# Optimization experiments

Measured on AMD Instinct MI355X. Metric: run time of the kernel, lower is better.

## Reference

```python
import jax, jax.numpy as jnp
import numpy as np

OUT_F, IN_F, RANK, GROUP = 8192, 8192, 16, 128
N_GROUPS = OUT_F * IN_F // GROUP  # 524288
TOKENS = 256


def block_dequantize_2bit(weight_q2, weight_norm):
    """weight_q2: [n_groups, GROUP//4] int (uint8 values), weight_norm: [n_groups, 1] fp16.
    Each byte packs 4 two-bit codes little-endian (code k in bits 2k..2k+1).
    Code q in {0..3} dequantizes to ((q/3)*2 - 1) * norm."""
    shifts = jnp.array([0, 2, 4, 6], dtype=jnp.int32)
    q = (weight_q2[:, :, None] >> shifts) & 3          # [n_groups, GROUP//4, 4]
    q = q.reshape(weight_q2.shape[0], -1).astype(jnp.float32)  # [n_groups, GROUP]
    return (q * (2.0 / 3.0) - 1.0) * weight_norm.astype(jnp.float32)


def setup_inputs() -> dict:
    key = jax.random.key(0)
    ks = jax.random.split(key, 6)
    x = jax.random.normal(ks[0], (TOKENS, IN_F), dtype=jnp.float32)
    weight_q2 = jax.random.randint(ks[1], (N_GROUPS, GROUP // 4), 0, 256, dtype=jnp.int32)
    weight_norm = jax.random.uniform(ks[2], (N_GROUPS, 1), dtype=jnp.float16, minval=0.01, maxval=1.0)
    bias = jax.random.normal(ks[3], (OUT_F,), dtype=jnp.float32)
    lora_a = jax.random.normal(ks[4], (RANK, IN_F), dtype=jnp.float32) * 0.02
    lora_b = jax.random.normal(ks[5], (OUT_F, RANK), dtype=jnp.float32) * 0.02
    return {"x": x, "weight_q2": weight_q2, "weight_norm": weight_norm,
            "bias": bias, "lora_a": lora_a, "lora_b": lora_b}


def reference(x, weight_q2, weight_norm, bias, lora_a, lora_b):
    x_f32 = x.astype(jnp.float32)
    W = block_dequantize_2bit(weight_q2, weight_norm).reshape(OUT_F, IN_F)  # fp32 [out, in]
    base_out = x_f32 @ W.T + bias                       # [tokens, out]
    lora_out = (x_f32 @ lora_a.T) @ lora_b.T            # [tokens, out]
    return (base_out + lora_out).astype(x.dtype)
```

## Files before the change

kernel.cpp:

```cpp
#include <hip/hip_runtime.h>
#include <hip/hip_fp16.h>

typedef unsigned int u32;
typedef unsigned short u16;
typedef _Float16 f16x8 __attribute__((ext_vector_type(8)));
typedef float f32x4 __attribute__((ext_vector_type(4)));

#define OUT_F 8192
#define IN_F 8192
#define TOKENS 256
#define N_GROUPS 524288
#define SPLITK 8
#define KSPAN (IN_F / SPLITK)
#define KT (KSPAN / 64)

#define XB_OFF 0
#define T_OFF ((size_t)TOKENS * IN_F * 2)
#define NF_OFF (T_OFF + 65536)
#define PART_OFF (NF_OFF + (size_t)N_GROUPS * 2)
#define PART_BYTES ((size_t)SPLITK * TOKENS * OUT_F * 4)
#define WS_NEED (PART_OFF + PART_BYTES)

#define GLOAD16(g, l)                                                        \
  __builtin_amdgcn_global_load_lds(                                          \
      (const __attribute__((address_space(1))) void*)(g),                    \
      (__attribute__((address_space(3))) void*)(l), 16, 0, 0)

__device__ __forceinline__ u32 hm2(u32 a, __half2 s) {
  return __builtin_bit_cast(u32, __hmul2(__builtin_bit_cast(__half2, a), s));
}

__global__ __launch_bounds__(256) void prep(const void* __restrict__ wn,
                                            __half* __restrict__ nf,
                                            const float* __restrict__ x,
                                            const float* __restrict__ la,
                                            u16* __restrict__ xb,
                                            float* __restrict__ t) {
  int tid = threadIdx.x;
  if (blockIdx.x < 512) {
    __shared__ int votes[3];
    if (tid < 3) votes[tid] = 0;
    __syncthreads();
    const u16* pu = (const u16*)wn;
    const u32* pw = (const u32*)wn;
    int v16 = 0, vbf = 0, vf = 0;
    for (int i = tid; i < 2048; i += 256) {
      u16 u = pu[i];
      float h = __half2float(__builtin_bit_cast(__half, u));
      float b = __builtin_bit_cast(float, ((u32)u) << 16);
      if (h > 0.008f && h < 1.002f) v16++;
      if (b > 0.008f && b < 1.002f) vbf++;
    }
    for (int i = tid; i < 1024; i += 256) {
      float f = __builtin_bit_cast(float, pw[i]);
      if (f > 0.008f && f < 1.002f) vf++;
    }
    atomicAdd(&votes[0], v16);
    atomicAdd(&votes[1], vbf);
    atomicAdd(&votes[2], vf);
    __syncthreads();
    int a16 = votes[0], abf = votes[1], af32 = 2 * votes[2];
    int mode = (a16 >= abf && a16 >= af32) ? 0 : (abf >= af32 ? 1 : 2);
#pragma unroll
    for (int i = 0; i < 4; ++i) {
      int g = blockIdx.x * 1024 + i * 256 + tid;
      float v;
      if (mode == 0) v = __half2float(((const __half*)wn)[g]);
      else if (mode == 1) v = __builtin_bit_cast(float, ((u32)((const u16*)wn)[g]) << 16);
      else v = ((const float*)wn)[g];
      nf[g] = __float2half(v);
    }
    return;
  }
  int b2 = blockIdx.x - 512;
  int m = b2 & 255;
  int half = b2 >> 8;
  const float4* xr = (const float4*)(x + (size_t)m * IN_F);
  u32* xbr = (u32*)(xb + (size_t)m * IN_F);
  float pl[16];
#pragma unroll
  for (int r = 0; r < 16; ++r) pl[r] = 0.f;
#pragma unroll
  for (int it = 0; it < 4; ++it) {
    int k4 = half * 1024 + it * 256 + tid;
    float4 xv = xr[k4];
    u32 p0 = __builtin_bit_cast(u32, __float22half2_rn(make_float2(xv.x, xv.y)));
    u32 p1 = __builtin_bit_cast(u32, __float22half2_rn(make_float2(xv.z, xv.w)));
    ((uint2*)xbr)[k4] = make_uint2(p0, p1);
#pragma unroll
    for (int r = 0; r < 16; ++r) {
      const float4 av = ((const float4*)(la + (size_t)r * IN_F))[k4];
      pl[r] = fmaf(xv.x, av.x, pl[r]);
      pl[r] = fmaf(xv.y, av.y, pl[r]);
      pl[r] = fmaf(xv.z, av.z, pl[r]);
      pl[r] = fmaf(xv.w, av.w, pl[r]);
    }
  }
#pragma unroll
  for (int r = 0; r < 16; ++r) {
    float v = pl[r];
#pragma unroll
    for (int d = 32; d > 0; d >>= 1) v += __shfl_xor(v, d);
    pl[r] = v;
  }
  __shared__ float red[4][16];
  int wave = tid >> 6, lane = tid & 63;
  if (lane == 0) {
#pragma unroll
    for (int r = 0; r < 16; ++r) red[wave][r] = pl[r];
  }
  __syncthreads();
  if (tid < 16)
    t[((size_t)half * TOKENS + m) * 16 + tid] =
        red[0][tid] + red[1][tid] + red[2][tid] + red[3][tid];
}

__global__ __launch_bounds__(256) void prep2(const float* __restrict__ t,
                                             const float* __restrict__ lb,
                                             const float* __restrict__ bias,
                                             float* __restrict__ out) {
  __shared__ float tS[16 * 16];
  int tid = threadIdx.x;
  int n = blockIdx.x * 256 + tid;
  int mbase = blockIdx.y * 16;
  if (tid < 64) {
    float4 a = ((const float4*)(t + (size_t)mbase * 16))[tid];
    float4 b = ((const float4*)(t + (size_t)TOKENS * 16 + (size_t)mbase * 16))[tid];
    ((float4*)tS)[tid] = make_float4(a.x + b.x, a.y + b.y, a.z + b.z, a.w + b.w);
  }
  const float4* lbp = (const float4*)(lb + (size_t)n * 16);
  float4 b0 = lbp[0], b1 = lbp[1], b2 = lbp[2], b3 = lbp[3];
  float bv = bias[n];
  __syncthreads();
#pragma unroll
  for (int mm = 0; mm < 16; ++mm) {
    const float* tr = &tS[mm * 16];
    float a = bv;
    a += tr[0] * b0.x + tr[1] * b0.y + tr[2] * b0.z + tr[3] * b0.w;
    a += tr[4] * b1.x + tr[5] * b1.y + tr[6] * b1.z + tr[7] * b1.w;
    a += tr[8] * b2.x + tr[9] * b2.y + tr[10] * b2.z + tr[11] * b2.w;
    a += tr[12] * b3.x + tr[13] * b3.y + tr[14] * b3.z + tr[15] * b3.w;
    out[(size_t)(mbase + mm) * OUT_F + n] = a;
  }
}

__global__ __launch_bounds__(256) void finish(const float* __restrict__ t,
                                              const float* __restrict__ lb,
                                              const float* __restrict__ bias,
                                              const float* __restrict__ part,
                                              float* __restrict__ out) {
  __shared__ float tS[16 * 16];
  int tid = threadIdx.x;
  int n = blockIdx.x * 256 + tid;
  int mbase = blockIdx.y * 16;
  if (tid < 64) {
    float4 a = ((const float4*)(t + (size_t)mbase * 16))[tid];
    float4 b = ((const float4*)(t + (size_t)TOKENS * 16 + (size_t)mbase * 16))[tid];
    ((float4*)tS)[tid] = make_float4(a.x + b.x, a.y + b.y, a.z + b.z, a.w + b.w);
  }
  const float4* lbp = (const float4*)(lb + (size_t)n * 16);
  float4 b0 = lbp[0], b1 = lbp[1], b2 = lbp[2], b3 = lbp[3];
  float bv = bias[n];
  __syncthreads();
#pragma unroll
  for (int mm = 0; mm < 16; ++mm) {
    const float* tr = &tS[mm * 16];
    float a = bv;
    a += tr[0] * b0.x + tr[1] * b0.y + tr[2] * b0.z + tr[3] * b0.w;
    a += tr[4] * b1.x + tr[5] * b1.y + tr[6] * b1.z + tr[7] * b1.w;
    a += tr[8] * b2.x + tr[9] * b2.y + tr[10] * b2.z + tr[11] * b2.w;
    a += tr[12] * b3.x + tr[13] * b3.y + tr[14] * b3.z + tr[15] * b3.w;
    size_t base = (size_t)(mbase + mm) * OUT_F + n;
#pragma unroll
    for (int kz = 0; kz < SPLITK; ++kz)
      a += part[(size_t)kz * TOKENS * OUT_F + base];
    out[base] = a;
  }
}

__global__ __launch_bounds__(256, 3) void gemm_q2(const u16* __restrict__ xb,
                                                  const int* __restrict__ wq,
                                                  const __half* __restrict__ wn,
                                                  float* __restrict__ dst,
                                                  int mode) {
  __shared__ __align__(16) u16 As[2][128 * 64];
  __shared__ __align__(16) u16 Bs[128 * 64];
  __shared__ uint2 lut[256];

  int tid = threadIdx.x;
  int n0 = blockIdx.x * 128;
  int m0 = blockIdx.y * 128;
  int kz = blockIdx.z;
  int kbase = kz * KSPAN;

  {
    int b = tid;
    float v0 = (float)(b & 3) * (2.f / 3.f) - 1.f;
    float v1 = (float)((b >> 2) & 3) * (2.f / 3.f) - 1.f;
    float v2 = (float)((b >> 4) & 3) * (2.f / 3.f) - 1.f;
    float v3 = (float)((b >> 6) & 3) * (2.f / 3.f) - 1.f;
    u32 lo = __builtin_bit_cast(u32, __float22half2_rn(make_float2(v0, v1)));
    u32 hi = __builtin_bit_cast(u32, __float22half2_rn(make_float2(v2, v3)));
    lut[b] = make_uint2(lo, hi);
  }

  int wave = tid >> 6, lane = tid & 63;
  int quad = lane >> 4, l15 = lane & 15;
  int mo = (wave & 1) * 64, no = (wave >> 1) * 64;

  int aslot[4];
  const u16* ag[4];
#pragma unroll
  for (int i = 0; i < 4; ++i) {
    int s = tid + i * 256;
    int mm = s >> 3, c = s & 7;
    int cl = c ^ (mm & 7);
    aslot[i] = s;
    ag[i] = xb + (size_t)(m0 + mm) * IN_F + kbase + cl * 8;
  }

  int bn = tid >> 1, h = tid & 1;
  const char* gB = (const char*)wq + (size_t)(n0 + bn) * IN_F + kbase + h * 32;
  const __half* wnp = wn + (size_t)(n0 + bn) * 64 + kz * (KSPAN / 128);

  f32x4 zero4 = {0.f, 0.f, 0.f, 0.f};
  f32x4 acc[4][4];
#pragma unroll
  for (int i = 0; i < 4; ++i)
#pragma unroll
    for (int j = 0; j < 4; ++j) acc[i][j] = zero4;

#pragma unroll
  for (int i = 0; i < 4; ++i) GLOAD16(ag[i], &((uint4*)As[0])[aslot[i]]);
  int4 pb0 = *(const int4*)(gB);
  int4 pb1 = *(const int4*)(gB + 16);
  __half pn = wnp[0];
  int cur = 0;

#pragma unroll 1
  for (int kt = 0; kt < KT; ++kt) {
    __syncthreads();

    {
      __half2 nh = __half2half2(pn);
      int vv[8] = {pb0.x, pb0.y, pb0.z, pb0.w, pb1.x, pb1.y, pb1.z, pb1.w};
      u32 uu[16];
#pragma unroll
      for (int e = 0; e < 8; ++e) {
        uint2 lv = lut[vv[e] & 255];
        uu[2 * e] = hm2(lv.x, nh);
        uu[2 * e + 1] = hm2(lv.y, nh);
      }
      uint4* Bw = (uint4*)Bs;
#pragma unroll
      for (int cc = 0; cc < 4; ++cc) {
        int pc = (h * 4 + cc) ^ (bn & 7);
        Bw[bn * 8 + pc] = make_uint4(uu[4 * cc], uu[4 * cc + 1], uu[4 * cc + 2], uu[4 * cc + 3]);
      }
    }

    if (kt < KT - 1) {
      int ko = (kt + 1) * 64;
#pragma unroll
      for (int i = 0; i < 4; ++i)
        GLOAD16(ag[i] + ko, &((uint4*)As[cur ^ 1])[aslot[i]]);
      pb0 = *(const int4*)(gB + ko);
      pb1 = *(const int4*)(gB + ko + 16);
      pn = wnp[(kt + 1) >> 1];
    }

    asm volatile("s_waitcnt lgkmcnt(0)" ::: "memory");
    __builtin_amdgcn_s_barrier();
    asm volatile("" ::: "memory");

    const uint4* Ar = (const uint4*)As[cur];
#pragma unroll
    for (int ks = 0; ks < 2; ++ks) {
      f16x8 af[4], bf[4];
#pragma unroll
      for (int mt = 0; mt < 4; ++mt) {
        int row = mo + mt * 16 + l15;
        int pc = (ks * 4 + quad) ^ (row & 7);
        af[mt] = __builtin_bit_cast(f16x8, Ar[row * 8 + pc]);
      }
#pragma unroll
      for (int nt = 0; nt < 4; ++nt) {
        int row = no + nt * 16 + l15;
        int pc = (ks * 4 + quad) ^ (row & 7);
        bf[nt] = __builtin_bit_cast(f16x8, ((const uint4*)Bs)[row * 8 + pc]);
      }
#pragma unroll
      for (int mt = 0; mt < 4; ++mt)
#pragma unroll
        for (int nt = 0; nt < 4; ++nt)
          acc[mt][nt] = __builtin_amdgcn_mfma_f32_16x16x32_f16(af[mt], bf[nt], acc[mt][nt], 0, 0, 0);
    }
    cur ^= 1;
  }

  if (mode) {
    float* pp = dst + (size_t)kz * TOKENS * OUT_F;
#pragma unroll
    for (int mt = 0; mt < 4; ++mt)
#pragma unroll
      for (int nt = 0; nt < 4; ++nt)
#pragma unroll
        for (int r = 0; r < 4; ++r) {
          int mm = m0 + mo + mt * 16 + quad * 4 + r;
          int nn = n0 + no + nt * 16 + l15;
          pp[(size_t)mm * OUT_F + nn] = acc[mt][nt][r];
        }
  } else {
#pragma unroll
    for (int mt = 0; mt < 4; ++mt)
#pragma unroll
      for (int nt = 0; nt < 4; ++nt)
#pragma unroll
        for (int r = 0; r < 4; ++r) {
          int mm = m0 + mo + mt * 16 + quad * 4 + r;
          int nn = n0 + no + nt * 16 + l15;
          atomicAdd(&dst[(size_t)mm * OUT_F + nn], acc[mt][nt][r]);
        }
  }
}

extern "C" void kernel_launch(void* const* d_in, const int* in_sizes, int n_in,
                              void* d_out, int out_size, void* d_ws, size_t ws_size,
                              hipStream_t stream) {
  (void)in_sizes; (void)n_in; (void)out_size;
  const float* x = (const float*)d_in[0];
  const int* wq = (const int*)d_in[1];
  const void* wn_raw = d_in[2];
  const float* bias = (const float*)d_in[3];
  const float* la = (const float*)d_in[4];
  const float* lb = (const float*)d_in[5];
  float* out = (float*)d_out;

  u16* xb = (u16*)((char*)d_ws + XB_OFF);
  float* t = (float*)((char*)d_ws + T_OFF);
  __half* nf = (__half*)((char*)d_ws + NF_OFF);
  float* part = (float*)((char*)d_ws + PART_OFF);
  int usep = ws_size >= WS_NEED;

  prep<<<1024, 256, 0, stream>>>(wn_raw, nf, x, la, xb, t);
  if (usep) {
    gemm_q2<<<dim3(OUT_F / 128, TOKENS / 128, SPLITK), 256, 0, stream>>>(xb, wq, nf, part, 1);
    finish<<<dim3(OUT_F / 256, TOKENS / 16), 256, 0, stream>>>(t, lb, bias, part, out);
  } else {
    prep2<<<dim3(OUT_F / 256, TOKENS / 16), 256, 0, stream>>>(t, lb, bias, out);
    gemm_q2<<<dim3(OUT_F / 128, TOKENS / 128, SPLITK), 256, 0, stream>>>(xb, wq, nf, out, 0);
  }
}
```

Measured before the change: 185.8 us.

## Triple-buffer A tiles with vmcnt waits, halve split-K, re-tile LoRA prep

The GEMM loop now keeps three LDS buffers for the activation tile. Loads are issued two k-steps ahead and waited on with vmcnt, replacing the earlier double buffer that drained every step. Split-K drops from 8 to 4, which halves the partial-sum traffic in finish, and launch bounds are relaxed to 2 waves per SIMD because LDS use grows. The LoRA prep kernel now gives each block 16 tokens over one eighth of K, producing 8 slices that prep2 and finish sum. The loop issues a wrapped, redundant load on the last iterations, and the lower occupancy may expose more latency.

```diff
diff --git a/kernel.cpp b/kernel.cpp
--- a/kernel.cpp
+++ b/kernel.cpp
@@ -10,13 +10,15 @@
 #define IN_F 8192
 #define TOKENS 256
 #define N_GROUPS 524288
-#define SPLITK 8
+#define SPLITK 4
 #define KSPAN (IN_F / SPLITK)
 #define KT (KSPAN / 64)
+#define TSLICES 8
 
 #define XB_OFF 0
 #define T_OFF ((size_t)TOKENS * IN_F * 2)
-#define NF_OFF (T_OFF + 65536)
+#define T_BYTES ((size_t)TSLICES * TOKENS * 16 * 4)
+#define NF_OFF (T_OFF + T_BYTES)
 #define PART_OFF (NF_OFF + (size_t)N_GROUPS * 2)
 #define PART_BYTES ((size_t)SPLITK * TOKENS * OUT_F * 4)
 #define WS_NEED (PART_OFF + PART_BYTES)
@@ -73,16 +75,18 @@
     return;
   }
   int b2 = blockIdx.x - 512;
-  int m = b2 & 255;
-  int half = b2 >> 8;
+  int kq = b2 & 7;
+  int mg = b2 >> 3;
+  int tm = tid >> 4, tk = tid & 15;
+  int m = mg * 16 + tm;
   const float4* xr = (const float4*)(x + (size_t)m * IN_F);
   u32* xbr = (u32*)(xb + (size_t)m * IN_F);
   float pl[16];
 #pragma unroll
   for (int r = 0; r < 16; ++r) pl[r] = 0.f;
 #pragma unroll
-  for (int it = 0; it < 4; ++it) {
-    int k4 = half * 1024 + it * 256 + tid;
+  for (int it = 0; it < 16; ++it) {
+    int k4 = kq * 256 + it * 16 + tk;
     float4 xv = xr[k4];
     u32 p0 = __builtin_bit_cast(u32, __float22half2_rn(make_float2(xv.x, xv.y)));
     u32 p1 = __builtin_bit_cast(u32, __float22half2_rn(make_float2(xv.z, xv.w)));
@@ -100,19 +104,14 @@
   for (int r = 0; r < 16; ++r) {
     float v = pl[r];
 #pragma unroll
-    for (int d = 32; d > 0; d >>= 1) v += __shfl_xor(v, d);
+    for (int d = 8; d > 0; d >>= 1) v += __shfl_xor(v, d);
     pl[r] = v;
   }
-  __shared__ float red[4][16];
-  int wave = tid >> 6, lane = tid & 63;
-  if (lane == 0) {
-#pragma unroll
-    for (int r = 0; r < 16; ++r) red[wave][r] = pl[r];
-  }
-  __syncthreads();
-  if (tid < 16)
-    t[((size_t)half * TOKENS + m) * 16 + tid] =
-        red[0][tid] + red[1][tid] + red[2][tid] + red[3][tid];
+  if (tk == 0) {
+    float* tp = t + ((size_t)kq * TOKENS + m) * 16;
+#pragma unroll
+    for (int r = 0; r < 16; ++r) tp[r] = pl[r];
+  }
 }
 
 __global__ __launch_bounds__(256) void prep2(const float* __restrict__ t,
@@ -124,9 +123,13 @@
   int n = blockIdx.x * 256 + tid;
   int mbase = blockIdx.y * 16;
   if (tid < 64) {
-    float4 a = ((const float4*)(t + (size_t)mbase * 16))[tid];
-    float4 b = ((const float4*)(t + (size_t)TOKENS * 16 + (size_t)mbase * 16))[tid];
-    ((float4*)tS)[tid] = make_float4(a.x + b.x, a.y + b.y, a.z + b.z, a.w + b.w);
+    float4 s = make_float4(0.f, 0.f, 0.f, 0.f);
+#pragma unroll
+    for (int sl = 0; sl < TSLICES; ++sl) {
+      float4 a = ((const float4*)(t + (size_t)sl * TOKENS * 16 + (size_t)mbase * 16))[tid];
+      s.x += a.x; s.y += a.y; s.z += a.z; s.w += a.w;
+    }
+    ((float4*)tS)[tid] = s;
   }
   const float4* lbp = (const float4*)(lb + (size_t)n * 16);
   float4 b0 = lbp[0], b1 = lbp[1], b2 = lbp[2], b3 = lbp[3];
@@ -154,9 +157,13 @@
   int n = blockIdx.x * 256 + tid;
   int mbase = blockIdx.y * 16;
   if (tid < 64) {
-    float4 a = ((const float4*)(t + (size_t)mbase * 16))[tid];
-    float4 b = ((const float4*)(t + (size_t)TOKENS * 16 + (size_t)mbase * 16))[tid];
-    ((float4*)tS)[tid] = make_float4(a.x + b.x, a.y + b.y, a.z + b.z, a.w + b.w);
+    float4 s = make_float4(0.f, 0.f, 0.f, 0.f);
+#pragma unroll
+    for (int sl = 0; sl < TSLICES; ++sl) {
+      float4 a = ((const float4*)(t + (size_t)sl * TOKENS * 16 + (size_t)mbase * 16))[tid];
+      s.x += a.x; s.y += a.y; s.z += a.z; s.w += a.w;
+    }
+    ((float4*)tS)[tid] = s;
   }
   const float4* lbp = (const float4*)(lb + (size_t)n * 16);
   float4 b0 = lbp[0], b1 = lbp[1], b2 = lbp[2], b3 = lbp[3];
@@ -178,12 +185,14 @@
   }
 }
 
-__global__ __launch_bounds__(256, 3) void gemm_q2(const u16* __restrict__ xb,
+__global__ __launch_bounds__(256, 2) void gemm_q2(const u16* __restrict__ xb,
                                                   const int* __restrict__ wq,
                                                   const __half* __restrict__ wn,
                                                   float* __restrict__ dst,
                                                   int mode) {
-  __shared__ __align__(16) u16 As[2][128 * 64];
+  __shared__ __align__(16) u16 As0[128 * 64];
+  __shared__ __align__(16) u16 As1[128 * 64];
+  __shared__ __align__(16) u16 As2[128 * 64];
   __shared__ __align__(16) u16 Bs[128 * 64];
   __shared__ uint2 lut[256];
 
@@ -230,73 +239,99 @@
 #pragma unroll
     for (int j = 0; j < 4; ++j) acc[i][j] = zero4;
 
-#pragma unroll
-  for (int i = 0; i < 4; ++i) GLOAD16(ag[i], &((uint4*)As[0])[aslot[i]]);
-  int4 pb0 = *(const int4*)(gB);
-  int4 pb1 = *(const int4*)(gB + 16);
-  __half pn = wnp[0];
-  int cur = 0;
+  u16* r0 = As0;
+  u16* r1 = As1;
+  u16* r2 = As2;
+
+  int4 pbX0, pbX1, pbY0, pbY1;
+  __half pnX, pnY;
+
+  __builtin_amdgcn_sched_barrier(0);
+#pragma unroll
+  for (int i = 0; i < 4; ++i) GLOAD16(ag[i], &((uint4*)r0)[aslot[i]]);
+  pbX0 = *(const int4*)(gB);
+  pbX1 = *(const int4*)(gB + 16);
+  pnX = wnp[0];
+  __builtin_amdgcn_sched_barrier(0);
+#pragma unroll
+  for (int i = 0; i < 4; ++i) GLOAD16(ag[i] + 64, &((uint4*)r1)[aslot[i]]);
+  pbY0 = *(const int4*)(gB + 64);
+  pbY1 = *(const int4*)(gB + 80);
+  pnY = wnp[0];
+  __builtin_amdgcn_sched_barrier(0);
+  asm volatile("s_waitcnt lgkmcnt(0)" ::: "memory");
+
+#define BODY(KTV, PB0, PB1, PN, RCUR, RDMA)                                    \
+  do {                                                                         \
+    asm volatile("s_waitcnt vmcnt(7)" ::: "memory");                           \
+    __builtin_amdgcn_s_barrier();                                              \
+    asm volatile("" ::: "memory");                                             \
+    __builtin_amdgcn_sched_barrier(0);                                         \
+    {                                            \
+      __half2 nh = __half2half2(PN);                                           \
+      int vv[8] = {PB0.x, PB0.y, PB0.z, PB0.w, PB1.x, PB1.y, PB1.z, PB1.w};    \
+      u32 uu[16];                                                              \
+      _Pragma("unroll") for (int e = 0; e < 8; ++e) {                          \
+        uint2 lv = lut[vv[e] & 255];                                           \
+        uu[2 * e] = hm2(lv.x, nh);                                             \
+        uu[2 * e + 1] = hm2(lv.y, nh);                                         \
+      }                                                                        \
+      uint4* Bw = (uint4*)Bs;                                                  \
+      _Pragma("unroll") for (int cc = 0; cc < 4; ++cc) {                       \
+        int pc = (h * 4 + cc) ^ (bn & 7);                                      \
+        Bw[bn * 8 + pc] =                                                      \
+            make_uint4(uu[4 * cc], uu[4 * cc + 1], uu[4 * cc + 2], uu[4 * cc + 3]); \
+      }                                                                        \
+    }                                                                          \
+    __builtin_amdgcn_sched_barrier(0);                                         \
+    {     \
+      int kn = (KTV) + 2;                                                      \
+      if (kn >= KT) kn = 0;                                                    \
+      int ko = kn * 64;                                                        \
+      GLOAD16(ag[0] + ko, &((uint4*)RDMA)[aslot[0]]);                          \
+      GLOAD16(ag[1] + ko, &((uint4*)RDMA)[aslot[1]]);                          \
+      GLOAD16(ag[2] + ko, &((uint4*)RDMA)[aslot[2]]);                          \
+      GLOAD16(ag[3] + ko, &((uint4*)RDMA)[aslot[3]]);                          \
+      PB0 = *(const int4*)(gB + ko);                                           \
+      PB1 = *(const int4*)(gB + ko + 16);                                      \
+      PN = wnp[kn >> 1];                                                       \
+    }                                                                          \
+    __builtin_amdgcn_sched_barrier(0);                                         \
+    asm volatile("s_waitcnt lgkmcnt(0)" ::: "memory");                         \
+    __builtin_amdgcn_s_barrier();                                              \
+    asm volatile("" ::: "memory");                                             \
+    __builtin_amdgcn_sched_barrier(0);                                         \
+    {              \
+      const uint4* Ar = (const uint4*)(RCUR);                                  \
+      _Pragma("unroll") for (int ks = 0; ks < 2; ++ks) {                       \
+        f16x8 af[4], bf[4];                                                    \
+        _Pragma("unroll") for (int mt = 0; mt < 4; ++mt) {                     \
+          int row = mo + mt * 16 + l15;                                        \
+          int pc = (ks * 4 + quad) ^ (row & 7);                                \
+          af[mt] = __builtin_bit_cast(f16x8, Ar[row * 8 + pc]);                \
+        }                                                                      \
+        _Pragma("unroll") for (int nt = 0; nt < 4; ++nt) {                     \
+          int row = no + nt * 16 + l15;                                        \
+          int pc = (ks * 4 + quad) ^ (row & 7);                                \
+          bf[nt] = __builtin_bit_cast(f16x8, ((const uint4*)Bs)[row * 8 + pc]);\
+        }                                                                      \
+        _Pragma("unroll") for (int mt = 0; mt < 4; ++mt)                       \
+            _Pragma("unroll") for (int nt = 0; nt < 4; ++nt)                   \
+                acc[mt][nt] = __builtin_amdgcn_mfma_f32_16x16x32_f16(          \
+                    af[mt], bf[nt], acc[mt][nt], 0, 0, 0);                     \
+      }                                                                        \
+    }                                                                          \
+  } while (0)
 
 #pragma unroll 1
-  for (int kt = 0; kt < KT; ++kt) {
-    __syncthreads();
-
-    {
-      __half2 nh = __half2half2(pn);
-      int vv[8] = {pb0.x, pb0.y, pb0.z, pb0.w, pb1.x, pb1.y, pb1.z, pb1.w};
-      u32 uu[16];
-#pragma unroll
-      for (int e = 0; e < 8; ++e) {
-        uint2 lv = lut[vv[e] & 255];
-        uu[2 * e] = hm2(lv.x, nh);
-        uu[2 * e + 1] = hm2(lv.y, nh);
-      }
-      uint4* Bw = (uint4*)Bs;
-#pragma unroll
-      for (int cc = 0; cc < 4; ++cc) {
-        int pc = (h * 4 + cc) ^ (bn & 7);
-        Bw[bn * 8 + pc] = make_uint4(uu[4 * cc], uu[4 * cc + 1], uu[4 * cc + 2], uu[4 * cc + 3]);
-      }
-    }
-
-    if (kt < KT - 1) {
-      int ko = (kt + 1) * 64;
-#pragma unroll
-      for (int i = 0; i < 4; ++i)
-        GLOAD16(ag[i] + ko, &((uint4*)As[cur ^ 1])[aslot[i]]);
-      pb0 = *(const int4*)(gB + ko);
-      pb1 = *(const int4*)(gB + ko + 16);
-      pn = wnp[(kt + 1) >> 1];
-    }
-
-    asm volatile("s_waitcnt lgkmcnt(0)" ::: "memory");
-    __builtin_amdgcn_s_barrier();
-    asm volatile("" ::: "memory");
-
-    const uint4* Ar = (const uint4*)As[cur];
-#pragma unroll
-    for (int ks = 0; ks < 2; ++ks) {
-      f16x8 af[4], bf[4];
-#pragma unroll
-      for (int mt = 0; mt < 4; ++mt) {
-        int row = mo + mt * 16 + l15;
-        int pc = (ks * 4 + quad) ^ (row & 7);
-        af[mt] = __builtin_bit_cast(f16x8, Ar[row * 8 + pc]);
-      }
-#pragma unroll
-      for (int nt = 0; nt < 4; ++nt) {
-        int row = no + nt * 16 + l15;
-        int pc = (ks * 4 + quad) ^ (row & 7);
-        bf[nt] = __builtin_bit_cast(f16x8, ((const uint4*)Bs)[row * 8 + pc]);
-      }
-#pragma unroll
-      for (int mt = 0; mt < 4; ++mt)
-#pragma unroll
-        for (int nt = 0; nt < 4; ++nt)
-          acc[mt][nt] = __builtin_amdgcn_mfma_f32_16x16x32_f16(af[mt], bf[nt], acc[mt][nt], 0, 0, 0);
-    }
-    cur ^= 1;
-  }
+  for (int p = 0; p < KT / 2; ++p) {
+    int kt = 2 * p;
+    BODY(kt, pbX0, pbX1, pnX, r0, r2);
+    { u16* tmp = r0; r0 = r1; r1 = r2; r2 = tmp; }
+    BODY(kt + 1, pbY0, pbY1, pnY, r0, r2);
+    { u16* tmp = r0; r0 = r1; r1 = r2; r2 = tmp; }
+  }
+#undef BODY
 
   if (mode) {
     float* pp = dst + (size_t)kz * TOKENS * OUT_F;
@@ -342,7 +377,7 @@
   float* part = (float*)((char*)d_ws + PART_OFF);
   int usep = ws_size >= WS_NEED;
 
-  prep<<<1024, 256, 0, stream>>>(wn_raw, nf, x, la, xb, t);
+  prep<<<640, 256, 0, stream>>>(wn_raw, nf, x, la, xb, t);
   if (usep) {
     gemm_q2<<<dim3(OUT_F / 128, TOKENS / 128, SPLITK), 256, 0, stream>>>(xb, wq, nf, part, 1);
     finish<<<dim3(OUT_F / 256, TOKENS / 16), 256, 0, stream>>>(t, lb, bias, part, out);
```

After: 191.9 us. 3.3% more time.

## Double-buffer dequantized weights and software-pipeline loads with MFMA, halve split-K

Applied to the files above, without the earlier changes.

Restructures the GEMM main loop so the B tile is double-buffered in LDS. The dequantization of the next k-tile runs while MFMAs consume the current tile, and weight registers are prefetched two tiles ahead, leaving a single barrier per iteration. It also raises MFMA wave priority with s_setprio and cuts SPLITK from 8 to 4, which reduces partial-sum traffic in the reduce step. The extra LDS buffer lowers occupancy from 3 to 2 blocks per CU, and the loop issues wrap-around prefetch loads on the last iterations.

```diff
diff --git a/kernel.cpp b/kernel.cpp
--- a/kernel.cpp
+++ b/kernel.cpp
@@ -10,7 +10,7 @@
 #define IN_F 8192
 #define TOKENS 256
 #define N_GROUPS 524288
-#define SPLITK 8
+#define SPLITK 4
 #define KSPAN (IN_F / SPLITK)
 #define KT (KSPAN / 64)
 
@@ -178,13 +178,13 @@
   }
 }
 
-__global__ __launch_bounds__(256, 3) void gemm_q2(const u16* __restrict__ xb,
+__global__ __launch_bounds__(256, 2) void gemm_q2(const u16* __restrict__ xb,
                                                   const int* __restrict__ wq,
                                                   const __half* __restrict__ wn,
                                                   float* __restrict__ dst,
                                                   int mode) {
   __shared__ __align__(16) u16 As[2][128 * 64];
-  __shared__ __align__(16) u16 Bs[128 * 64];
+  __shared__ __align__(16) u16 Bs[2][128 * 64];
   __shared__ uint2 lut[256];
 
   int tid = threadIdx.x;
@@ -230,73 +230,86 @@
 #pragma unroll
     for (int j = 0; j < 4; ++j) acc[i][j] = zero4;
 
+#define DEQ(PB0, PB1, PN, BUF)                                                 \
+  {                                                                            \
+    __half2 nh = __half2half2(PN);                                             \
+    int vv[8] = {PB0.x, PB0.y, PB0.z, PB0.w, PB1.x, PB1.y, PB1.z, PB1.w};      \
+    u32 uu[16];                                                                \
+    _Pragma("unroll") for (int e = 0; e < 8; ++e) {                            \
+      uint2 lv = lut[vv[e] & 255];                                             \
+      uu[2 * e] = hm2(lv.x, nh);                                               \
+      uu[2 * e + 1] = hm2(lv.y, nh);                                           \
+    }                                                                          \
+    uint4* Bw = (uint4*)Bs[BUF];                                               \
+    _Pragma("unroll") for (int cc = 0; cc < 4; ++cc) {                         \
+      int pc = (h * 4 + cc) ^ (bn & 7);                                        \
+      Bw[bn * 8 + pc] =                                                        \
+          make_uint4(uu[4 * cc], uu[4 * cc + 1], uu[4 * cc + 2], uu[4 * cc + 3]); \
+    }                                                                          \
+  }
+
+  int4 pbX0, pbX1, pbY0, pbY1;
+  __half pnX, pnY;
+
 #pragma unroll
   for (int i = 0; i < 4; ++i) GLOAD16(ag[i], &((uint4*)As[0])[aslot[i]]);
-  int4 pb0 = *(const int4*)(gB);
-  int4 pb1 = *(const int4*)(gB + 16);
-  __half pn = wnp[0];
-  int cur = 0;
+  pbX0 = *(const int4*)(gB);
+  pbX1 = *(const int4*)(gB + 16);
+  pnX = wnp[0];
+  __syncthreads();
+  DEQ(pbX0, pbX1, pnX, 0);
+  pbY0 = *(const int4*)(gB + 64);
+  pbY1 = *(const int4*)(gB + 80);
+  pnY = wnp[0];
+  __syncthreads();
+
+#define BODY(KTV, CUR, DB0, DB1, DN, LB0, LB1, LN)                             \
+  do {                                                                         \
+    int kn1 = (KTV) + 1; if (kn1 >= KT) kn1 = 0;                               \
+    int kn2 = (KTV) + 2; if (kn2 >= KT) kn2 = 0;                               \
+    int ko1 = kn1 * 64, ko2 = kn2 * 64;                                        \
+    GLOAD16(ag[0] + ko1, &((uint4*)As[(CUR) ^ 1])[aslot[0]]);                  \
+    GLOAD16(ag[1] + ko1, &((uint4*)As[(CUR) ^ 1])[aslot[1]]);                  \
+    GLOAD16(ag[2] + ko1, &((uint4*)As[(CUR) ^ 1])[aslot[2]]);                  \
+    GLOAD16(ag[3] + ko1, &((uint4*)As[(CUR) ^ 1])[aslot[3]]);                  \
+    LB0 = *(const int4*)(gB + ko2);                                            \
+    LB1 = *(const int4*)(gB + ko2 + 16);                                       \
+    LN = wnp[kn2 >> 1];                                                        \
+    DEQ(DB0, DB1, DN, (CUR) ^ 1);                                              \
+    {                                                                          \
+      const uint4* Ar = (const uint4*)As[CUR];                                 \
+      const uint4* Br = (const uint4*)Bs[CUR];                                 \
+      _Pragma("unroll") for (int ks = 0; ks < 2; ++ks) {                       \
+        f16x8 af[4], bf[4];                                                    \
+        _Pragma("unroll") for (int mt = 0; mt < 4; ++mt) {                     \
+          int row = mo + mt * 16 + l15;                                        \
+          int pc = (ks * 4 + quad) ^ (row & 7);                                \
+          af[mt] = __builtin_bit_cast(f16x8, Ar[row * 8 + pc]);                \
+        }                                                                      \
+        _Pragma("unroll") for (int nt = 0; nt < 4; ++nt) {                     \
+          int row = no + nt * 16 + l15;                                        \
+          int pc = (ks * 4 + quad) ^ (row & 7);                                \
+          bf[nt] = __builtin_bit_cast(f16x8, Br[row * 8 + pc]);                \
+        }                                                                      \
+        __builtin_amdgcn_s_setprio(1);                                         \
+        _Pragma("unroll") for (int mt = 0; mt < 4; ++mt)                       \
+            _Pragma("unroll") for (int nt = 0; nt < 4; ++nt)                   \
+                acc[mt][nt] = __builtin_amdgcn_mfma_f32_16x16x32_f16(          \
+                    af[mt], bf[nt], acc[mt][nt], 0, 0, 0);                     \
+        __builtin_amdgcn_s_setprio(0);                                         \
+      }                                                                        \
+    }                                                                          \
+    __syncthreads();                                                           \
+  } while (0)
 
 #pragma unroll 1
-  for (int kt = 0; kt < KT; ++kt) {
-    __syncthreads();
-
-    {
-      __half2 nh = __half2half2(pn);
-      int vv[8] = {pb0.x, pb0.y, pb0.z, pb0.w, pb1.x, pb1.y, pb1.z, pb1.w};
-      u32 uu[16];
-#pragma unroll
-      for (int e = 0; e < 8; ++e) {
-        uint2 lv = lut[vv[e] & 255];
-        uu[2 * e] = hm2(lv.x, nh);
-        uu[2 * e + 1] = hm2(lv.y, nh);
-      }
-      uint4* Bw = (uint4*)Bs;
-#pragma unroll
-      for (int cc = 0; cc < 4; ++cc) {
-        int pc = (h * 4 + cc) ^ (bn & 7);
-        Bw[bn * 8 + pc] = make_uint4(uu[4 * cc], uu[4 * cc + 1], uu[4 * cc + 2], uu[4 * cc + 3]);
-      }
-    }
-
-    if (kt < KT - 1) {
-      int ko = (kt + 1) * 64;
-#pragma unroll
-      for (int i = 0; i < 4; ++i)
-        GLOAD16(ag[i] + ko, &((uint4*)As[cur ^ 1])[aslot[i]]);
-      pb0 = *(const int4*)(gB + ko);
-      pb1 = *(const int4*)(gB + ko + 16);
-      pn = wnp[(kt + 1) >> 1];
-    }
-
-    asm volatile("s_waitcnt lgkmcnt(0)" ::: "memory");
-    __builtin_amdgcn_s_barrier();
-    asm volatile("" ::: "memory");
-
-    const uint4* Ar = (const uint4*)As[cur];
-#pragma unroll
-    for (int ks = 0; ks < 2; ++ks) {
-      f16x8 af[4], bf[4];
-#pragma unroll
-      for (int mt = 0; mt < 4; ++mt) {
-        int row = mo + mt * 16 + l15;
-        int pc = (ks * 4 + quad) ^ (row & 7);
-        af[mt] = __builtin_bit_cast(f16x8, Ar[row * 8 + pc]);
-      }
-#pragma unroll
-      for (int nt = 0; nt < 4; ++nt) {
-        int row = no + nt * 16 + l15;
-        int pc = (ks * 4 + quad) ^ (row & 7);
-        bf[nt] = __builtin_bit_cast(f16x8, ((const uint4*)Bs)[row * 8 + pc]);
-      }
-#pragma unroll
-      for (int mt = 0; mt < 4; ++mt)
-#pragma unroll
-        for (int nt = 0; nt < 4; ++nt)
-          acc[mt][nt] = __builtin_amdgcn_mfma_f32_16x16x32_f16(af[mt], bf[nt], acc[mt][nt], 0, 0, 0);
-    }
-    cur ^= 1;
-  }
+  for (int p = 0; p < KT / 2; ++p) {
+    int kt = 2 * p;
+    BODY(kt, 0, pbY0, pbY1, pnY, pbX0, pbX1, pnX);
+    BODY(kt + 1, 1, pbX0, pbX1, pnX, pbY0, pbY1, pnY);
+  }
+#undef BODY
+#undef DEQ
 
   if (mode) {
     float* pp = dst + (size_t)kz * TOKENS * OUT_F;
```

Result: faster. 176.0 us (-5.3%).

## Load GEMM fragments straight from global memory, dequantize via exponent bit trick

Applied to the files above, without the earlier changes.

The GEMM drops LDS staging and barriers. Each wave loads its A and packed 2-bit B fragments directly from global memory into registers, with B prefetched one k-step ahead. Dequantization swaps the LDS lookup table for an fp16 exponent bit trick followed by a single hfma2 per pair. Split-K goes from 8 to 4 and launch bounds from 3 to 2 blocks per SM. This removes LDS traffic and synchronization, but it loses cross-wave reuse of A and B, so the same data is re-read from global or cache, and there are fewer blocks in flight.

```diff
diff --git a/kernel.cpp b/kernel.cpp
--- a/kernel.cpp
+++ b/kernel.cpp
@@ -10,7 +10,7 @@
 #define IN_F 8192
 #define TOKENS 256
 #define N_GROUPS 524288
-#define SPLITK 8
+#define SPLITK 4
 #define KSPAN (IN_F / SPLITK)
 #define KT (KSPAN / 64)
 
@@ -20,15 +20,6 @@
 #define PART_OFF (NF_OFF + (size_t)N_GROUPS * 2)
 #define PART_BYTES ((size_t)SPLITK * TOKENS * OUT_F * 4)
 #define WS_NEED (PART_OFF + PART_BYTES)
-
-#define GLOAD16(g, l)                                                        \
-  __builtin_amdgcn_global_load_lds(                                          \
-      (const __attribute__((address_space(1))) void*)(g),                    \
-      (__attribute__((address_space(3))) void*)(l), 16, 0, 0)
-
-__device__ __forceinline__ u32 hm2(u32 a, __half2 s) {
-  return __builtin_bit_cast(u32, __hmul2(__builtin_bit_cast(__half2, a), s));
-}
 
 __global__ __launch_bounds__(256) void prep(const void* __restrict__ wn,
                                             __half* __restrict__ nf,
@@ -178,50 +169,44 @@
   }
 }
 
-__global__ __launch_bounds__(256, 3) void gemm_q2(const u16* __restrict__ xb,
+__device__ __forceinline__ __half2 h2u(u32 x) { return __builtin_bit_cast(__half2, x); }
+
+__device__ __forceinline__ f16x8 bfrag(u32 bA, u32 bB, __half2 s, __half2 c) {
+  u32 w[4];
+  w[0] = __builtin_bit_cast(u32, __hfma2(h2u(0x40004000u | ((bA & 3u) << 8) | ((bA & 0xCu) << 22)), s, c));
+  w[1] = __builtin_bit_cast(u32, __hfma2(h2u(0x40004000u | ((bA & 0x30u) << 4) | ((bA & 0xC0u) << 18)), s, c));
+  w[2] = __builtin_bit_cast(u32, __hfma2(h2u(0x40004000u | ((bB & 3u) << 8) | ((bB & 0xCu) << 22)), s, c));
+  w[3] = __builtin_bit_cast(u32, __hfma2(h2u(0x40004000u | ((bB & 0x30u) << 4) | ((bB & 0xC0u) << 18)), s, c));
+  uint4 p = make_uint4(w[0], w[1], w[2], w[3]);
+  return __builtin_bit_cast(f16x8, p);
+}
+
+__global__ __launch_bounds__(256, 2) void gemm_q2(const u16* __restrict__ xb,
                                                   const int* __restrict__ wq,
                                                   const __half* __restrict__ wn,
                                                   float* __restrict__ dst,
                                                   int mode) {
-  __shared__ __align__(16) u16 As[2][128 * 64];
-  __shared__ __align__(16) u16 Bs[128 * 64];
-  __shared__ uint2 lut[256];
-
   int tid = threadIdx.x;
   int n0 = blockIdx.x * 128;
   int m0 = blockIdx.y * 128;
   int kz = blockIdx.z;
-  int kbase = kz * KSPAN;
-
-  {
-    int b = tid;
-    float v0 = (float)(b & 3) * (2.f / 3.f) - 1.f;
-    float v1 = (float)((b >> 2) & 3) * (2.f / 3.f) - 1.f;
-    float v2 = (float)((b >> 4) & 3) * (2.f / 3.f) - 1.f;
-    float v3 = (float)((b >> 6) & 3) * (2.f / 3.f) - 1.f;
-    u32 lo = __builtin_bit_cast(u32, __float22half2_rn(make_float2(v0, v1)));
-    u32 hi = __builtin_bit_cast(u32, __float22half2_rn(make_float2(v2, v3)));
-    lut[b] = make_uint2(lo, hi);
-  }
-
   int wave = tid >> 6, lane = tid & 63;
-  int quad = lane >> 4, l15 = lane & 15;
+  int q = lane >> 4, l15 = lane & 15;
   int mo = (wave & 1) * 64, no = (wave >> 1) * 64;
 
-  int aslot[4];
-  const u16* ag[4];
-#pragma unroll
-  for (int i = 0; i < 4; ++i) {
-    int s = tid + i * 256;
-    int mm = s >> 3, c = s & 7;
-    int cl = c ^ (mm & 7);
-    aslot[i] = s;
-    ag[i] = xb + (size_t)(m0 + mm) * IN_F + kbase + cl * 8;
-  }
-
-  int bn = tid >> 1, h = tid & 1;
-  const char* gB = (const char*)wq + (size_t)(n0 + bn) * IN_F + kbase + h * 32;
-  const __half* wnp = wn + (size_t)(n0 + bn) * 64 + kz * (KSPAN / 128);
+  const u16* ap[4];
+#pragma unroll
+  for (int mt = 0; mt < 4; ++mt)
+    ap[mt] = xb + (size_t)(m0 + mo + mt * 16 + l15) * IN_F + (size_t)kz * KSPAN + q * 16;
+
+  const int* bp[4];
+  const __half* np[4];
+#pragma unroll
+  for (int nt = 0; nt < 4; ++nt) {
+    int row = n0 + no + nt * 16 + l15;
+    bp[nt] = wq + (size_t)row * (IN_F / 4) + (size_t)kz * (KSPAN / 4) + q * 4;
+    np[nt] = wn + (size_t)row * (IN_F / 128) + (size_t)kz * (KSPAN / 128);
+  }
 
   f32x4 zero4 = {0.f, 0.f, 0.f, 0.f};
   f32x4 acc[4][4];
@@ -230,73 +215,69 @@
 #pragma unroll
     for (int j = 0; j < 4; ++j) acc[i][j] = zero4;
 
-#pragma unroll
-  for (int i = 0; i < 4; ++i) GLOAD16(ag[i], &((uint4*)As[0])[aslot[i]]);
-  int4 pb0 = *(const int4*)(gB);
-  int4 pb1 = *(const int4*)(gB + 16);
-  __half pn = wnp[0];
-  int cur = 0;
+  int4 cbX[4], cbY[4];
+  __half nr[4];
+  __half2 s2[4], c2[4];
+#pragma unroll
+  for (int nt = 0; nt < 4; ++nt) cbX[nt] = *(const int4*)(bp[nt]);
+#pragma unroll
+  for (int nt = 0; nt < 4; ++nt) nr[nt] = np[nt][0];
+#pragma unroll
+  for (int nt = 0; nt < 4; ++nt) {
+    float f = __half2float(nr[nt]);
+    s2[nt] = __float2half2_rn(f * (4.f / 3.f));
+    c2[nt] = __float2half2_rn(f * (-11.f / 3.f));
+  }
+
+#define COMPUTE(KTV, CB)                                                       \
+  do {                                                                         \
+    uint4 av0[4], av1[4];                                                      \
+    _Pragma("unroll") for (int mt = 0; mt < 4; ++mt)                           \
+        av0[mt] = *(const uint4*)(ap[mt] + (KTV) * 64);                        \
+    _Pragma("unroll") for (int mt = 0; mt < 4; ++mt)                           \
+        av1[mt] = *(const uint4*)(ap[mt] + (KTV) * 64 + 8);                    \
+    f16x8 bf0[4], bf1[4];                                                      \
+    _Pragma("unroll") for (int nt = 0; nt < 4; ++nt)                           \
+        bf0[nt] = bfrag((u32)CB[nt].x, (u32)CB[nt].y, s2[nt], c2[nt]);         \
+    _Pragma("unroll") for (int nt = 0; nt < 4; ++nt)                           \
+        bf1[nt] = bfrag((u32)CB[nt].z, (u32)CB[nt].w, s2[nt], c2[nt]);         \
+    __builtin_amdgcn_s_setprio(1);                                             \
+    _Pragma("unroll") for (int mt = 0; mt < 4; ++mt) {                         \
+      f16x8 a0 = __builtin_bit_cast(f16x8, av0[mt]);                           \
+      _Pragma("unroll") for (int nt = 0; nt < 4; ++nt)                         \
+          acc[mt][nt] = __builtin_amdgcn_mfma_f32_16x16x32_f16(                \
+              a0, bf0[nt], acc[mt][nt], 0, 0, 0);                              \
+    }                                                                          \
+    _Pragma("unroll") for (int mt = 0; mt < 4; ++mt) {                         \
+      f16x8 a1 = __builtin_bit_cast(f16x8, av1[mt]);                           \
+      _Pragma("unroll") for (int nt = 0; nt < 4; ++nt)                         \
+          acc[mt][nt] = __builtin_amdgcn_mfma_f32_16x16x32_f16(                \
+              a1, bf1[nt], acc[mt][nt], 0, 0, 0);                              \
+    }                                                                          \
+    __builtin_amdgcn_s_setprio(0);                                             \
+  } while (0)
 
 #pragma unroll 1
-  for (int kt = 0; kt < KT; ++kt) {
-    __syncthreads();
-
-    {
-      __half2 nh = __half2half2(pn);
-      int vv[8] = {pb0.x, pb0.y, pb0.z, pb0.w, pb1.x, pb1.y, pb1.z, pb1.w};
-      u32 uu[16];
-#pragma unroll
-      for (int e = 0; e < 8; ++e) {
-        uint2 lv = lut[vv[e] & 255];
-        uu[2 * e] = hm2(lv.x, nh);
-        uu[2 * e + 1] = hm2(lv.y, nh);
-      }
-      uint4* Bw = (uint4*)Bs;
-#pragma unroll
-      for (int cc = 0; cc < 4; ++cc) {
-        int pc = (h * 4 + cc) ^ (bn & 7);
-        Bw[bn * 8 + pc] = make_uint4(uu[4 * cc], uu[4 * cc + 1], uu[4 * cc + 2], uu[4 * cc + 3]);
-      }
-    }
-
-    if (kt < KT - 1) {
-      int ko = (kt + 1) * 64;
-#pragma unroll
-      for (int i = 0; i < 4; ++i)
-        GLOAD16(ag[i] + ko, &((uint4*)As[cur ^ 1])[aslot[i]]);
-      pb0 = *(const int4*)(gB + ko);
-      pb1 = *(const int4*)(gB + ko + 16);
-      pn = wnp[(kt + 1) >> 1];
-    }
-
-    asm volatile("s_waitcnt lgkmcnt(0)" ::: "memory");
-    __builtin_amdgcn_s_barrier();
-    asm volatile("" ::: "memory");
-
-    const uint4* Ar = (const uint4*)As[cur];
-#pragma unroll
-    for (int ks = 0; ks < 2; ++ks) {
-      f16x8 af[4], bf[4];
-#pragma unroll
-      for (int mt = 0; mt < 4; ++mt) {
-        int row = mo + mt * 16 + l15;
-        int pc = (ks * 4 + quad) ^ (row & 7);
-        af[mt] = __builtin_bit_cast(f16x8, Ar[row * 8 + pc]);
-      }
-#pragma unroll
-      for (int nt = 0; nt < 4; ++nt) {
-        int row = no + nt * 16 + l15;
-        int pc = (ks * 4 + quad) ^ (row & 7);
-        bf[nt] = __builtin_bit_cast(f16x8, ((const uint4*)Bs)[row * 8 + pc]);
-      }
-#pragma unroll
-      for (int mt = 0; mt < 4; ++mt)
-#pragma unroll
-        for (int nt = 0; nt < 4; ++nt)
-          acc[mt][nt] = __builtin_amdgcn_mfma_f32_16x16x32_f16(af[mt], bf[nt], acc[mt][nt], 0, 0, 0);
-    }
-    cur ^= 1;
-  }
+  for (int p = 0; p < KT / 2; ++p) {
+    int ktA = 2 * p, ktB = 2 * p + 1;
+    int kq = (p + 1 < KT / 2) ? (p + 1) : 0;
+    int kn = (ktB + 1 < KT) ? (ktB + 1) : 0;
+#pragma unroll
+    for (int nt = 0; nt < 4; ++nt) cbY[nt] = *(const int4*)(bp[nt] + ktB * 16);
+#pragma unroll
+    for (int nt = 0; nt < 4; ++nt) nr[nt] = np[nt][kq];
+    COMPUTE(ktA, cbX);
+#pragma unroll
+    for (int nt = 0; nt < 4; ++nt) cbX[nt] = *(const int4*)(bp[nt] + kn * 16);
+    COMPUTE(ktB, cbY);
+#pragma unroll
+    for (int nt = 0; nt < 4; ++nt) {
+      float f = __half2float(nr[nt]);
+      s2[nt] = __float2half2_rn(f * (4.f / 3.f));
+      c2[nt] = __float2half2_rn(f * (-11.f / 3.f));
+    }
+  }
+#undef COMPUTE
 
   if (mode) {
     float* pp = dst + (size_t)kz * TOKENS * OUT_F;
@@ -306,7 +287,7 @@
       for (int nt = 0; nt < 4; ++nt)
 #pragma unroll
         for (int r = 0; r < 4; ++r) {
-          int mm = m0 + mo + mt * 16 + quad * 4 + r;
+          int mm = m0 + mo + mt * 16 + q * 4 + r;
           int nn = n0 + no + nt * 16 + l15;
           pp[(size_t)mm * OUT_F + nn] = acc[mt][nt][r];
         }
@@ -317,7 +298,7 @@
       for (int nt = 0; nt < 4; ++nt)
 #pragma unroll
         for (int r = 0; r < 4; ++r) {
-          int mm = m0 + mo + mt * 16 + quad * 4 + r;
+          int mm = m0 + mo + mt * 16 + q * 4 + r;
           int nn = n0 + no + nt * 16 + l15;
           atomicAdd(&dst[(size_t)mm * OUT_F + nn], acc[mt][nt][r]);
         }
```

Measured after the change: 221.4 us. 19.2% more time.
